# Kernel optimization log

Measured on AMD Instinct MI355X. Metric: run time of the kernel, lower is better.

## Reference

```python
import jax, jax.numpy as jnp
import numpy as np

IN_CH = 32
OUT_CH = 32
M1, M2 = 32, 32
BS, H, W = 8, 256, 256


def setup_inputs() -> dict:
    key = jax.random.key(0)
    kx, kk = jax.random.split(key)
    x = jax.random.normal(kx, (BS, IN_CH, H, W), dtype=jnp.float32)
    # reset_parameters: randn * (1/(in_ch*out_ch)) + 1
    scale = 1.0 / (IN_CH * OUT_CH)
    kernel = jax.random.normal(kk, (2, 1, OUT_CH, M1, M2, 2), dtype=jnp.float32) * scale + 1.0
    r = jnp.float32(1.0)
    return {"x": x, "kernel": kernel, "r": r}


def reference(x, kernel, r):
    # view_as_complex: last dim of 2 -> complex, shape [2, 1, C, M1, M2]
    kc = (kernel[..., 0] + 1j * kernel[..., 1]).astype(jnp.complex64)
    # elementwise complex power kernel**r
    kc = jnp.power(kc, r)

    # forward 2D real FFT over spatial dims (ortho norm)
    x_ft = jnp.fft.rfftn(x, axes=(-2, -1), norm="ortho")  # [bs, C, H, W//2+1]
    Hf, Wr = x_ft.shape[-2], x_ft.shape[-1]
    n1 = min(Hf // 2, M1)
    n2 = min(Wr, M2)

    def mix(block, k):
        # fft over channel dim (-3), multiply by complex kernel, ifft back
        b = jnp.fft.fft(block, axis=-3, norm="ortho")
        b = b * k[..., :n1, :n2]
        return jnp.fft.ifft(b, axis=-3, norm="ortho")

    pos = mix(x_ft[..., :n1, :n2], kc[0])          # low positive freqs
    neg = mix(x_ft[..., Hf - n1:, :n2], kc[1])     # low negative freqs

    out_ft = jnp.zeros((x.shape[0], OUT_CH, Hf, Wr), dtype=jnp.complex64)
    out_ft = out_ft.at[..., :n1, :n2].set(pos)
    out_ft = out_ft.at[..., Hf - n1:, :n2].set(neg)

    # inverse real FFT back to spatial domain
    return jnp.fft.irfftn(out_ft, s=(x.shape[-2], x.shape[-1]), axes=(-2, -1), norm="ortho")
```

## Files before the change

kernel.cpp:

```cpp
#include <hip/hip_runtime.h>
#include <math.h>


#define TWO_PI 6.28318530717958647692f

__global__ __launch_bounds__(256) void kP(const float* __restrict__ kin,
                                          const float* __restrict__ rp,
                                          float2* __restrict__ kp) {
  const int i = blockIdx.x * 256 + threadIdx.x;
  const float r = rp[0];
  const float kr = kin[2 * i], ki = kin[2 * i + 1];
  const float m2 = fmaf(kr, kr, ki * ki);
  float2 o = make_float2(0.f, 0.f);
  if (m2 > 0.f) {
    const float lm = 0.5f * logf(m2);
    const float ang = atan2f(ki, kr);
    const float mag = expf(r * lm);
    float s, c;
    sincosf(r * ang, &s, &c);
    o = make_float2(mag * c, mag * s);
  }
  kp[i] = o;
}

__global__ __launch_bounds__(256) void kA(const float* __restrict__ x,
                                          float2* __restrict__ z1) {
  __shared__ float xs[8192];
  const int tid = threadIdx.x;
  const long row0 = (long)blockIdx.x * 32;
  const float* xg = x + row0 * 256;
  {
    const int xl = tid & 31, rq = tid >> 5;
    const float* xgr = xg + rq * 4 * 256 + xl;
#pragma unroll
    for (int cb = 0; cb < 8; ++cb) {
      const int xc = xl + 32 * cb;
      const float4 v = make_float4(xgr[32 * cb], xgr[32 * cb + 256],
                                   xgr[32 * cb + 512], xgr[32 * cb + 768]);
      *(float4*)(xs + xc * 32 + 4 * ((rq + xc) & 7)) = v;
    }
  }
  __syncthreads();
  const float RT = 0.70710678118654752440f;
#pragma unroll
  for (int k = 0; k < 4; ++k) {
    const int i = tid + (k << 8);
    const int x1 = i >> 5, r = i & 31;
    float* base = xs + x1 * 32 + ((r + 4 * x1) & 31);
    const float a0 = base[0],        a1 = base[1024],     a2 = base[2048];
    const float a3 = base[3 * 1024], a4 = base[4 * 1024], a5 = base[5 * 1024];
    const float a6 = base[6 * 1024], a7 = base[7 * 1024];
    const float t0 = a0 + a4, t1 = a0 - a4, t2 = a2 + a6, t3 = a2 - a6;
    const float u0 = a1 + a5, u1 = a1 - a5, u2 = a3 + a7, u3 = a3 - a7;
    const float E0 = t0 + t2, O0 = u0 + u2;
    const float d1 = RT * (u1 - u3), d2 = RT * (u1 + u3);
    base[0]        = E0 + O0;
    base[1024]     = E0 - O0;
    base[2 * 1024] = t1 + d1;
    base[3 * 1024] = -(t3 + d2);
    base[4 * 1024] = t0 - t2;
    base[5 * 1024] = -(u0 - u2);
    base[6 * 1024] = t1 - d1;
    base[7 * 1024] = t3 - d2;
  }
  __syncthreads();
  const int w = tid & 31;
  const int r0 = (tid >> 5) << 2;
  const int p = w & 7;
  int pr, pi;
  float si;
  if (p == 0)      { pr = 0;           pi = 0;      si = 0.f; }
  else if (p == 4) { pr = 1;           pi = 1;      si = 0.f; }
  else if (p < 4)  { pr = 2 * p;       pi = pr + 1; si = 1.f; }
  else             { pr = 2 * (8 - p); pi = pr + 1; si = -1.f; }
  const char* ur = (const char*)xs + pr * 4096;
  const char* ui = (const char*)xs + pi * 4096;
  const char* urp[8];
  const char* uip[8];
#pragma unroll
  for (int j = 0; j < 8; ++j) {
    const int off = 4 * ((r0 + 4 * j) & 31) + 128 * j;
    urp[j] = ur + off;
    uip[j] = ui + off;
  }
  float s1, c1;
  sincosf(-TWO_PI * (float)w / 256.0f, &s1, &c1);
  float pc = 1.f, ps = 0.f;
  float Cr0 = 0, Cr1 = 0, Cr2 = 0, Cr3 = 0;
  float Ci0 = 0, Ci1 = 0, Ci2 = 0, Ci3 = 0;
#pragma unroll
  for (int bq = 0; bq < 4; ++bq) {
#pragma unroll
    for (int j = 0; j < 8; ++j) {
      const float4 Fr = *(const float4*)(urp[j] + bq * 1024);
      const float4 Fi = *(const float4*)(uip[j] + bq * 1024);
      const float qs = si * ps, qc = si * pc;
      Cr0 = fmaf(Fr.x, pc, fmaf(-Fi.x, qs, Cr0));
      Ci0 = fmaf(Fr.x, ps, fmaf( Fi.x, qc, Ci0));
      Cr1 = fmaf(Fr.y, pc, fmaf(-Fi.y, qs, Cr1));
      Ci1 = fmaf(Fr.y, ps, fmaf( Fi.y, qc, Ci1));
      Cr2 = fmaf(Fr.z, pc, fmaf(-Fi.z, qs, Cr2));
      Ci2 = fmaf(Fr.z, ps, fmaf( Fi.z, qc, Ci2));
      Cr3 = fmaf(Fr.w, pc, fmaf(-Fi.w, qs, Cr3));
      Ci3 = fmaf(Fr.w, ps, fmaf( Fi.w, qc, Ci3));
      const float tn = fmaf(pc, c1, -ps * s1);
      ps = fmaf(pc, s1, ps * c1);
      pc = tn;
    }
  }
  float2* o = z1 + (row0 + r0) * 32 + w;
  o[0]  = make_float2(Cr0, Ci0);
  o[32] = make_float2(Cr1, Ci1);
  o[64] = make_float2(Cr2, Ci2);
  o[96] = make_float2(Cr3, Ci3);
}

__global__ __launch_bounds__(256) void kB1(float2* __restrict__ z1) {
  const int gt = blockIdx.x * 256 + threadIdx.x;
  const int w = gt & 31, y1 = (gt >> 5) & 31, bc = gt >> 10;
  float2* base = z1 + (long)bc * 8192 + y1 * 32 + w;
  float2 a[8];
#pragma unroll
  for (int j = 0; j < 8; ++j) a[j] = base[j * 1024];
  float2 t0 = make_float2(a[0].x + a[4].x, a[0].y + a[4].y);
  float2 t1 = make_float2(a[0].x - a[4].x, a[0].y - a[4].y);
  float2 t2 = make_float2(a[2].x + a[6].x, a[2].y + a[6].y);
  float2 t3 = make_float2(a[2].x - a[6].x, a[2].y - a[6].y);
  const float2 E0 = make_float2(t0.x + t2.x, t0.y + t2.y);
  const float2 E2 = make_float2(t0.x - t2.x, t0.y - t2.y);
  const float2 E1 = make_float2(t1.x + t3.y, t1.y - t3.x);
  const float2 E3 = make_float2(t1.x - t3.y, t1.y + t3.x);
  t0 = make_float2(a[1].x + a[5].x, a[1].y + a[5].y);
  t1 = make_float2(a[1].x - a[5].x, a[1].y - a[5].y);
  t2 = make_float2(a[3].x + a[7].x, a[3].y + a[7].y);
  t3 = make_float2(a[3].x - a[7].x, a[3].y - a[7].y);
  const float2 O0 = make_float2(t0.x + t2.x, t0.y + t2.y);
  const float2 O2 = make_float2(t0.x - t2.x, t0.y - t2.y);
  const float2 O1 = make_float2(t1.x + t3.y, t1.y - t3.x);
  const float2 O3 = make_float2(t1.x - t3.y, t1.y + t3.x);
  const float RT = 0.70710678118654752440f;
  const float2 B0 = O0;
  const float2 B1 = make_float2(RT * (O1.x + O1.y), RT * (O1.y - O1.x));
  const float2 B2 = make_float2(O2.y, -O2.x);
  const float2 B3 = make_float2(RT * (O3.y - O3.x), -RT * (O3.x + O3.y));
  base[0]        = make_float2(E0.x + B0.x, E0.y + B0.y);
  base[1 * 1024] = make_float2(E1.x + B1.x, E1.y + B1.y);
  base[2 * 1024] = make_float2(E2.x + B2.x, E2.y + B2.y);
  base[3 * 1024] = make_float2(E3.x + B3.x, E3.y + B3.y);
  base[4 * 1024] = make_float2(E0.x - B0.x, E0.y - B0.y);
  base[5 * 1024] = make_float2(E1.x - B1.x, E1.y - B1.y);
  base[6 * 1024] = make_float2(E2.x - B2.x, E2.y - B2.y);
  base[7 * 1024] = make_float2(E3.x - B3.x, E3.y - B3.y);
}

__global__ __launch_bounds__(256) void kB2(const float2* __restrict__ s,
                                           float2* __restrict__ z2) {
  const int bc = blockIdx.x >> 3, tq = blockIdx.x & 7;
  const int k = threadIdx.x >> 5, w = threadIdx.x & 31;
  const int t = tq * 8 + k;
  const int h = (t < 32) ? t : (192 + t);
  float sr, cr;
  sincosf(-TWO_PI * (float)h / 256.0f, &sr, &cr);
  const float2* src = s + (long)bc * 8192 + k * 1024 + w;
  float ar = 0.f, ai = 0.f;
  float pc = 1.f, ps = 0.f;
  for (int y1 = 0; y1 < 32; ++y1) {
    const float2 v = src[y1 * 32];
    ar = fmaf(v.x, pc, fmaf(-v.y, ps, ar));
    ai = fmaf(v.x, ps, fmaf( v.y, pc, ai));
    const float tn = fmaf(pc, cr, -ps * sr);
    ps = fmaf(pc, sr, ps * cr);
    pc = tn;
  }
  z2[(long)bc * 2048 + t * 32 + w] = make_float2(ar, ai);
}

__global__ __launch_bounds__(256) void kC(const float2* __restrict__ z2,
                                          const float2* __restrict__ kp,
                                          float2* __restrict__ g) {
  __shared__ float2 z2s[8 * 33];
  __shared__ float2 fk[8 * 33];
  __shared__ float2 tw[32];
  const int tid = threadIdx.x;
  if (tid < 32) {
    float s, c;
    sincosf(-TWO_PI * (float)tid / 32.0f, &s, &c);
    tw[tid] = make_float2(c, s);
  }
  const int m0 = blockIdx.x * 8;
  const int b = m0 >> 11;
  const int twi = m0 & 2047;
  const int t = twi >> 5;
  const int w0 = twi & 31;
  const int s_ = t >> 5, tm = t & 31;
  {
    const int ci = tid >> 3, wj = tid & 7;
    z2s[wj * 33 + ci] = z2[((long)(b * 32 + ci)) * 2048 + t * 32 + w0 + wj];
  }
  __syncthreads();
  const int m = tid & 7;
  {
    const int cf = tid >> 3;
    float fr = 0, fi = 0;
    int i0 = 0;
#pragma unroll 8
    for (int ci = 0; ci < 32; ++ci) {
      const float2 z = z2s[m * 33 + ci];
      const float2 t0 = tw[i0]; i0 = (i0 + cf) & 31;
      fr = fmaf(z.x, t0.x, fmaf(-z.y, t0.y, fr));
      fi = fmaf(z.x, t0.y, fmaf( z.y, t0.x, fi));
    }
    const float2 k0 = kp[((s_ * 32 + cf) * 32 + tm) * 32 + w0 + m];
    fk[m * 33 + cf] = make_float2(fr * k0.x - fi * k0.y, fr * k0.y + fi * k0.x);
  }
  __syncthreads();
  {
    const int co = tid >> 3;
    float gr = 0, gi = 0;
    int i0 = 0;
#pragma unroll 8
    for (int cf = 0; cf < 32; ++cf) {
      const float2 f = fk[m * 33 + cf];
      const float2 t0 = tw[i0]; i0 = (i0 + co) & 31;
      gr = fmaf(f.x, t0.x, fmaf( f.y, t0.y, gr));
      gi = fmaf(f.y, t0.x, fmaf(-f.x, t0.y, gi));
    }
    const float SC = 1.0f / 8192.0f;
    g[((long)(b * 32 + co)) * 2048 + t * 32 + w0 + m] = make_float2(gr * SC, gi * SC);
  }
}

__global__ __launch_bounds__(256) void kD1(const float2* __restrict__ g,
                                           float2* __restrict__ U) {
  const int bc = blockIdx.x >> 3, y1q = blockIdx.x & 7;
  const int p = threadIdx.x >> 5, w = threadIdx.x & 31;
  const float2* gb = g + (long)bc * 2048 + w;
  float2* ub = U + (long)bc * 8192 + p * 32 + w;
#pragma unroll
  for (int y1l = 0; y1l < 4; ++y1l) {
    const int y1 = y1q * 4 + y1l;
    float st, ct;
    sincosf(TWO_PI * (float)y1 / 32.0f, &st, &ct);
    float s1, c1;
    sincosf(TWO_PI * (float)((p * y1) & 255) / 256.0f, &s1, &c1);
    float s2, c2;
    sincosf(TWO_PI * (float)(((224 + p) * y1) & 255) / 256.0f, &s2, &c2);
    float ar = 0.f, ai = 0.f;
    float pc = c1, ps = s1, qc = c2, qs = s2;
#pragma unroll
    for (int j = 0; j < 4; ++j) {
      const float2 va = gb[(p + 8 * j) * 32];
      const float2 vb = gb[(32 + p + 8 * j) * 32];
      ar = fmaf(va.x, pc, fmaf(-va.y, ps, ar));
      ai = fmaf(va.x, ps, fmaf( va.y, pc, ai));
      ar = fmaf(vb.x, qc, fmaf(-vb.y, qs, ar));
      ai = fmaf(vb.x, qs, fmaf( vb.y, qc, ai));
      const float tn = fmaf(pc, ct, -ps * st);
      ps = fmaf(pc, st, ps * ct);
      pc = tn;
      const float tm2 = fmaf(qc, ct, -qs * st);
      qs = fmaf(qc, st, qs * ct);
      qc = tm2;
    }
    ub[y1 * 256] = make_float2(ar, ai);
  }
}

__global__ __launch_bounds__(256) void kDE(const float2* __restrict__ U,
                                           float* __restrict__ out) {
  __shared__ float2 tst[32 * 34];
  const int tid = threadIdx.x;
  const int bc = blockIdx.x >> 3, yq = blockIdx.x & 7;
  {
    const int y5 = tid >> 3, wq = tid & 7;
    const float* ub = (const float*)(U + (long)bc * 8192 + (long)y5 * 256 + wq * 4);
    float Tr[4] = {0.f, 0.f, 0.f, 0.f}, Ti[4] = {0.f, 0.f, 0.f, 0.f};
#pragma unroll
    for (int p = 0; p < 8; ++p) {
      float sp, cp;
      sincosf(TWO_PI * (float)((p * yq) & 7) / 8.0f, &sp, &cp);
      const float4 qa = *(const float4*)(ub + p * 64);
      const float4 qb = *(const float4*)(ub + p * 64 + 4);
      Tr[0] = fmaf(qa.x, cp, fmaf(-qa.y, sp, Tr[0]));
      Ti[0] = fmaf(qa.x, sp, fmaf( qa.y, cp, Ti[0]));
      Tr[1] = fmaf(qa.z, cp, fmaf(-qa.w, sp, Tr[1]));
      Ti[1] = fmaf(qa.z, sp, fmaf( qa.w, cp, Ti[1]));
      Tr[2] = fmaf(qb.x, cp, fmaf(-qb.y, sp, Tr[2]));
      Ti[2] = fmaf(qb.x, sp, fmaf( qb.y, cp, Ti[2]));
      Tr[3] = fmaf(qb.z, cp, fmaf(-qb.w, sp, Tr[3]));
      Ti[3] = fmaf(qb.z, sp, fmaf( qb.w, cp, Ti[3]));
    }
#pragma unroll
    for (int kk = 0; kk < 4; ++kk) {
      const int w = wq * 4 + kk;
      const float sc = w ? (2.0f / 256.0f) : (1.0f / 256.0f);
      tst[w * 34 + y5] = make_float2(Tr[kk] * sc, Ti[kk] * sc);
    }
  }
  __syncthreads();
  {
    const int xq = tid & 31;
    const int rh = tid >> 5;
    float sb, cb;
    sincosf(TWO_PI * (float)xq / 256.0f, &sb, &cb);
    const float RT = 0.70710678118654752440f;
    const float stc1 = RT * (cb - sb), sts1 = RT * (cb + sb);
    const float stc[4] = {cb, stc1, -sb, -sts1};
    const float sts[4] = {sb, sts1, cb, stc1};
    float C[4][4], S[4][4];
#pragma unroll
    for (int m = 0; m < 4; ++m)
#pragma unroll
      for (int j = 0; j < 4; ++j) { C[m][j] = 0.f; S[m][j] = 0.f; }
    float pc[4] = {1.f, 1.f, 1.f, 1.f}, ps[4] = {0.f, 0.f, 0.f, 0.f};
    const float* tbse = (const float*)tst + rh * 8;
#pragma unroll 2
    for (int w = 0; w < 32; ++w) {
      const float4 q0 = *(const float4*)(tbse + w * 68);
      const float4 q1 = *(const float4*)(tbse + w * 68 + 4);
#pragma unroll
      for (int m = 0; m < 4; ++m) {
        C[m][0] = fmaf(q0.x, pc[m], C[m][0]);
        S[m][0] = fmaf(q0.y, ps[m], S[m][0]);
        C[m][1] = fmaf(q0.z, pc[m], C[m][1]);
        S[m][1] = fmaf(q0.w, ps[m], S[m][1]);
        C[m][2] = fmaf(q1.x, pc[m], C[m][2]);
        S[m][2] = fmaf(q1.y, ps[m], S[m][2]);
        C[m][3] = fmaf(q1.z, pc[m], C[m][3]);
        S[m][3] = fmaf(q1.w, ps[m], S[m][3]);
        const float tn = fmaf(pc[m], stc[m], -ps[m] * sts[m]);
        ps[m] = fmaf(pc[m], sts[m], ps[m] * stc[m]);
        pc[m] = tn;
      }
    }
    const long rbase = (long)bc * 256 + yq * 32;
#pragma unroll
    for (int m = 0; m < 4; ++m) {
      const int xx = xq + 32 * m;
#pragma unroll
      for (int j = 0; j < 4; ++j) {
        const long row = rbase + rh * 4 + j;
        out[row * 256 + xx] = C[m][j] - S[m][j];
        out[row * 256 + ((256 - xx) & 255)] = C[m][j] + S[m][j];
      }
    }
    if (tid < 32) {
      float ae = 0.f, ao = 0.f;
#pragma unroll
      for (int k = 0; k < 16; ++k) {
        ae += tst[(2 * k) * 34 + tid].x;
        ao += tst[(2 * k + 1) * 34 + tid].x;
      }
      out[(rbase + tid) * 256 + 128] = ae - ao;
    }
  }
}

extern "C" void kernel_launch(void* const* d_in, const int* in_sizes, int n_in,
                              void* d_out, int out_size, void* d_ws, size_t ws_size,
                              hipStream_t stream) {
  const float* x = (const float*)d_in[0];
  const float* kin = (const float*)d_in[1];
  const float* rp = (const float*)d_in[2];
  float* out = (float*)d_out;
  char* ws = (char*)d_ws;

  float2* z1 = (float2*)(ws);
  float2* z2 = (float2*)(ws + (16ull << 20));
  float2* kp = (float2*)(ws + (24ull << 20));
  float2* g  = (float2*)(ws);
  float2* U  = (float2*)(ws + (4ull << 20));

  kP<<<256, 256, 0, stream>>>(kin, rp, kp);
  kA<<<2048, 256, 0, stream>>>(x, z1);
  kB1<<<1024, 256, 0, stream>>>(z1);
  kB2<<<2048, 256, 0, stream>>>(z1, z2);
  kC<<<2048, 256, 0, stream>>>(z2, kp, g);
  kD1<<<2048, 256, 0, stream>>>(g, U);
  kDE<<<2048, 256, 0, stream>>>(U, out);
}
```

Before: 202.9 us.

## Split row DFT into radix-8 butterfly pass and truncated twiddle pass

```diff
diff --git a/kernel.cpp b/kernel.cpp
--- a/kernel.cpp
+++ b/kernel.cpp
@@ -21,6 +21,101 @@
     o = make_float2(mag * c, mag * s);
   }
   kp[i] = o;
+}
+
+__global__ __launch_bounds__(256) void kA1(const float* __restrict__ x,
+                                           float* __restrict__ F) {
+  const int tid = threadIdx.x;
+  const int x1 = tid & 31, rr = tid >> 5;
+  const long rb = blockIdx.x;
+  const float* xb = x + rb * 32 * 256 + x1;
+  float* Fb = F + rb * 8192 + x1;
+  const float RT = 0.70710678118654752440f;
+#pragma unroll
+  for (int k = 0; k < 4; ++k) {
+    const int rl = rr + 8 * k;
+    const float* xr = xb + rl * 256;
+    const float a0 = xr[0],   a1 = xr[32],  a2 = xr[64],  a3 = xr[96];
+    const float a4 = xr[128], a5 = xr[160], a6 = xr[192], a7 = xr[224];
+    const float t0 = a0 + a4, t1 = a0 - a4, t2 = a2 + a6, t3 = a2 - a6;
+    const float u0 = a1 + a5, u1 = a1 - a5, u2 = a3 + a7, u3 = a3 - a7;
+    const float E0 = t0 + t2, O0 = u0 + u2;
+    const float d1 = RT * (u1 - u3), d2 = RT * (u1 + u3);
+    float* Fo = Fb + rl * 32;
+    Fo[0]        = E0 + O0;
+    Fo[1024]     = E0 - O0;
+    Fo[2 * 1024] = t1 + d1;
+    Fo[3 * 1024] = -(t3 + d2);
+    Fo[4 * 1024] = t0 - t2;
+    Fo[5 * 1024] = -(u0 - u2);
+    Fo[6 * 1024] = t1 - d1;
+    Fo[7 * 1024] = t3 - d2;
+  }
+}
+
+__global__ __launch_bounds__(256) void kA2(const float* __restrict__ F,
+                                           float2* __restrict__ z1) {
+  const int tid = threadIdx.x;
+  const int w = tid & 31, rq = tid >> 5;
+  const long rb = blockIdx.x;
+  const int p = w & 7;
+  int pr, pi;
+  float si;
+  if (p == 0)      { pr = 0;           pi = 0;      si = 0.f; }
+  else if (p == 4) { pr = 1;           pi = 1;      si = 0.f; }
+  else if (p < 4)  { pr = 2 * p;       pi = pr + 1; si = 1.f; }
+  else             { pr = 2 * (8 - p); pi = pr + 1; si = -1.f; }
+  const float* Fr_ = F + rb * 8192 + pr * 1024 + rq * 128;
+  const float* Fi_ = F + rb * 8192 + pi * 1024 + rq * 128;
+  float s1, c1;
+  sincosf(-TWO_PI * (float)w / 256.0f, &s1, &c1);
+  float Pc[4], Ps[4];
+  Pc[0] = 1.f; Ps[0] = 0.f;
+  Pc[1] = c1;  Ps[1] = s1;
+  Pc[2] = fmaf(c1, c1, -s1 * s1);
+  Ps[2] = 2.f * c1 * s1;
+  Pc[3] = fmaf(Pc[2], c1, -Ps[2] * s1);
+  Ps[3] = fmaf(Pc[2], s1, Ps[2] * c1);
+  const float c4 = fmaf(Pc[3], c1, -Ps[3] * s1);
+  const float s4 = fmaf(Pc[3], s1, Ps[3] * c1);
+  float Cr[4] = {0.f, 0.f, 0.f, 0.f}, Ci[4] = {0.f, 0.f, 0.f, 0.f};
+#pragma unroll
+  for (int j = 0; j < 8; ++j) {
+    float4 fr[4], fi[4];
+#pragma unroll
+    for (int r = 0; r < 4; ++r) {
+      fr[r] = *(const float4*)(Fr_ + r * 32 + 4 * j);
+      fi[r] = *(const float4*)(Fi_ + r * 32 + 4 * j);
+    }
+    const float qs0 = si * Ps[0], qc0 = si * Pc[0];
+    const float qs1 = si * Ps[1], qc1 = si * Pc[1];
+    const float qs2 = si * Ps[2], qc2 = si * Pc[2];
+    const float qs3 = si * Ps[3], qc3 = si * Pc[3];
+#pragma unroll
+    for (int r = 0; r < 4; ++r) {
+      float cr = Cr[r], ci = Ci[r];
+      cr = fmaf(fr[r].x, Pc[0], fmaf(-fi[r].x, qs0, cr));
+      ci = fmaf(fr[r].x, Ps[0], fmaf( fi[r].x, qc0, ci));
+      cr = fmaf(fr[r].y, Pc[1], fmaf(-fi[r].y, qs1, cr));
+      ci = fmaf(fr[r].y, Ps[1], fmaf( fi[r].y, qc1, ci));
+      cr = fmaf(fr[r].z, Pc[2], fmaf(-fi[r].z, qs2, cr));
+      ci = fmaf(fr[r].z, Ps[2], fmaf( fi[r].z, qc2, ci));
+      cr = fmaf(fr[r].w, Pc[3], fmaf(-fi[r].w, qs3, cr));
+      ci = fmaf(fr[r].w, Ps[3], fmaf( fi[r].w, qc3, ci));
+      Cr[r] = cr; Ci[r] = ci;
+    }
+#pragma unroll
+    for (int m = 0; m < 4; ++m) {
+      const float tn = fmaf(Pc[m], c4, -Ps[m] * s4);
+      Ps[m] = fmaf(Pc[m], s4, Ps[m] * c4);
+      Pc[m] = tn;
+    }
+  }
+  float2* o = z1 + (rb * 32 + 4 * rq) * 32 + w;
+  o[0]  = make_float2(Cr[0], Ci[0]);
+  o[32] = make_float2(Cr[1], Ci[1]);
+  o[64] = make_float2(Cr[2], Ci[2]);
+  o[96] = make_float2(Cr[3], Ci[3]);
 }
 
 __global__ __launch_bounds__(256) void kA(const float* __restrict__ x,
@@ -365,17 +460,33 @@
   float* out = (float*)d_out;
   char* ws = (char*)d_ws;
 
-  float2* z1 = (float2*)(ws);
-  float2* z2 = (float2*)(ws + (16ull << 20));
-  float2* kp = (float2*)(ws + (24ull << 20));
-  float2* g  = (float2*)(ws);
-  float2* U  = (float2*)(ws + (4ull << 20));
-
-  kP<<<256, 256, 0, stream>>>(kin, rp, kp);
-  kA<<<2048, 256, 0, stream>>>(x, z1);
-  kB1<<<1024, 256, 0, stream>>>(z1);
-  kB2<<<2048, 256, 0, stream>>>(z1, z2);
-  kC<<<2048, 256, 0, stream>>>(z2, kp, g);
-  kD1<<<2048, 256, 0, stream>>>(g, U);
-  kDE<<<2048, 256, 0, stream>>>(U, out);
-}
+  if (ws_size >= (110ull << 20)) {
+    float*  F  = (float*)(ws);
+    float2* z1 = (float2*)(ws + (64ull << 20));
+    float2* z2 = (float2*)(ws + (80ull << 20));
+    float2* kp = (float2*)(ws + (88ull << 20));
+    float2* g  = (float2*)(ws + (89ull << 20));
+    float2* U  = (float2*)(ws + (93ull << 20));
+    kP<<<256, 256, 0, stream>>>(kin, rp, kp);
+    kA1<<<2048, 256, 0, stream>>>(x, F);
+    kA2<<<2048, 256, 0, stream>>>(F, z1);
+    kB1<<<1024, 256, 0, stream>>>(z1);
+    kB2<<<2048, 256, 0, stream>>>(z1, z2);
+    kC<<<2048, 256, 0, stream>>>(z2, kp, g);
+    kD1<<<2048, 256, 0, stream>>>(g, U);
+    kDE<<<2048, 256, 0, stream>>>(U, out);
+  } else {
+    float2* z1 = (float2*)(ws);
+    float2* z2 = (float2*)(ws + (16ull << 20));
+    float2* kp = (float2*)(ws + (24ull << 20));
+    float2* g  = (float2*)(ws);
+    float2* U  = (float2*)(ws + (4ull << 20));
+    kP<<<256, 256, 0, stream>>>(kin, rp, kp);
+    kA<<<2048, 256, 0, stream>>>(x, z1);
+    kB1<<<1024, 256, 0, stream>>>(z1);
+    kB2<<<2048, 256, 0, stream>>>(z1, z2);
+    kC<<<2048, 256, 0, stream>>>(z2, kp, g);
+    kD1<<<2048, 256, 0, stream>>>(g, U);
+    kDE<<<2048, 256, 0, stream>>>(U, out);
+  }
+}
```

New measurement: 261.8 us. 29.0% more time.

## Fuse radix-8 and DFT stages into LDS kernels, merge inverse stages

Applied to the files above, without the earlier changes.

```diff
diff --git a/kernel.cpp b/kernel.cpp
--- a/kernel.cpp
+++ b/kernel.cpp
@@ -115,64 +115,79 @@
   o[96] = make_float2(Cr3, Ci3);
 }
 
-__global__ __launch_bounds__(256) void kB1(float2* __restrict__ z1) {
-  const int gt = blockIdx.x * 256 + threadIdx.x;
-  const int w = gt & 31, y1 = (gt >> 5) & 31, bc = gt >> 10;
-  float2* base = z1 + (long)bc * 8192 + y1 * 32 + w;
-  float2 a[8];
-#pragma unroll
-  for (int j = 0; j < 8; ++j) a[j] = base[j * 1024];
-  float2 t0 = make_float2(a[0].x + a[4].x, a[0].y + a[4].y);
-  float2 t1 = make_float2(a[0].x - a[4].x, a[0].y - a[4].y);
-  float2 t2 = make_float2(a[2].x + a[6].x, a[2].y + a[6].y);
-  float2 t3 = make_float2(a[2].x - a[6].x, a[2].y - a[6].y);
-  const float2 E0 = make_float2(t0.x + t2.x, t0.y + t2.y);
-  const float2 E2 = make_float2(t0.x - t2.x, t0.y - t2.y);
-  const float2 E1 = make_float2(t1.x + t3.y, t1.y - t3.x);
-  const float2 E3 = make_float2(t1.x - t3.y, t1.y + t3.x);
-  t0 = make_float2(a[1].x + a[5].x, a[1].y + a[5].y);
-  t1 = make_float2(a[1].x - a[5].x, a[1].y - a[5].y);
-  t2 = make_float2(a[3].x + a[7].x, a[3].y + a[7].y);
-  t3 = make_float2(a[3].x - a[7].x, a[3].y - a[7].y);
-  const float2 O0 = make_float2(t0.x + t2.x, t0.y + t2.y);
-  const float2 O2 = make_float2(t0.x - t2.x, t0.y - t2.y);
-  const float2 O1 = make_float2(t1.x + t3.y, t1.y - t3.x);
-  const float2 O3 = make_float2(t1.x - t3.y, t1.y + t3.x);
+__global__ __launch_bounds__(256) void kB(const float2* __restrict__ z1,
+                                          float2* __restrict__ z2) {
+  __shared__ float2 zs[8192];
+  const int tid = threadIdx.x;
+  const int bc = blockIdx.x >> 1, th = blockIdx.x & 1;
+  {
+    const float4* s4 = (const float4*)(z1 + (long)bc * 8192);
+    float4* d4 = (float4*)zs;
+    for (int i = tid; i < 4096; i += 256) d4[i] = s4[i];
+  }
+  __syncthreads();
   const float RT = 0.70710678118654752440f;
-  const float2 B0 = O0;
-  const float2 B1 = make_float2(RT * (O1.x + O1.y), RT * (O1.y - O1.x));
-  const float2 B2 = make_float2(O2.y, -O2.x);
-  const float2 B3 = make_float2(RT * (O3.y - O3.x), -RT * (O3.x + O3.y));
-  base[0]        = make_float2(E0.x + B0.x, E0.y + B0.y);
-  base[1 * 1024] = make_float2(E1.x + B1.x, E1.y + B1.y);
-  base[2 * 1024] = make_float2(E2.x + B2.x, E2.y + B2.y);
-  base[3 * 1024] = make_float2(E3.x + B3.x, E3.y + B3.y);
-  base[4 * 1024] = make_float2(E0.x - B0.x, E0.y - B0.y);
-  base[5 * 1024] = make_float2(E1.x - B1.x, E1.y - B1.y);
-  base[6 * 1024] = make_float2(E2.x - B2.x, E2.y - B2.y);
-  base[7 * 1024] = make_float2(E3.x - B3.x, E3.y - B3.y);
-}
-
-__global__ __launch_bounds__(256) void kB2(const float2* __restrict__ s,
-                                           float2* __restrict__ z2) {
-  const int bc = blockIdx.x >> 3, tq = blockIdx.x & 7;
-  const int k = threadIdx.x >> 5, w = threadIdx.x & 31;
-  const int t = tq * 8 + k;
-  const int h = (t < 32) ? t : (192 + t);
-  float sr, cr;
-  sincosf(-TWO_PI * (float)h / 256.0f, &sr, &cr);
-  const float2* src = s + (long)bc * 8192 + k * 1024 + w;
-  float ar = 0.f, ai = 0.f;
-  float pc = 1.f, ps = 0.f;
+#pragma unroll
+  for (int e = 0; e < 4; ++e) {
+    float2* base = zs + tid + (e << 8);
+    float2 a[8];
+#pragma unroll
+    for (int j = 0; j < 8; ++j) a[j] = base[j * 1024];
+    float2 t0 = make_float2(a[0].x + a[4].x, a[0].y + a[4].y);
+    float2 t1 = make_float2(a[0].x - a[4].x, a[0].y - a[4].y);
+    float2 t2 = make_float2(a[2].x + a[6].x, a[2].y + a[6].y);
+    float2 t3 = make_float2(a[2].x - a[6].x, a[2].y - a[6].y);
+    const float2 E0 = make_float2(t0.x + t2.x, t0.y + t2.y);
+    const float2 E2 = make_float2(t0.x - t2.x, t0.y - t2.y);
+    const float2 E1 = make_float2(t1.x + t3.y, t1.y - t3.x);
+    const float2 E3 = make_float2(t1.x - t3.y, t1.y + t3.x);
+    t0 = make_float2(a[1].x + a[5].x, a[1].y + a[5].y);
+    t1 = make_float2(a[1].x - a[5].x, a[1].y - a[5].y);
+    t2 = make_float2(a[3].x + a[7].x, a[3].y + a[7].y);
+    t3 = make_float2(a[3].x - a[7].x, a[3].y - a[7].y);
+    const float2 O0 = make_float2(t0.x + t2.x, t0.y + t2.y);
+    const float2 O2 = make_float2(t0.x - t2.x, t0.y - t2.y);
+    const float2 O1 = make_float2(t1.x + t3.y, t1.y - t3.x);
+    const float2 O3 = make_float2(t1.x - t3.y, t1.y + t3.x);
+    const float2 B0 = O0;
+    const float2 B1 = make_float2(RT * (O1.x + O1.y), RT * (O1.y - O1.x));
+    const float2 B2 = make_float2(O2.y, -O2.x);
+    const float2 B3 = make_float2(RT * (O3.y - O3.x), -RT * (O3.x + O3.y));
+    base[0]        = make_float2(E0.x + B0.x, E0.y + B0.y);
+    base[1 * 1024] = make_float2(E1.x + B1.x, E1.y + B1.y);
+    base[2 * 1024] = make_float2(E2.x + B2.x, E2.y + B2.y);
+    base[3 * 1024] = make_float2(E3.x + B3.x, E3.y + B3.y);
+    base[4 * 1024] = make_float2(E0.x - B0.x, E0.y - B0.y);
+    base[5 * 1024] = make_float2(E1.x - B1.x, E1.y - B1.y);
+    base[6 * 1024] = make_float2(E2.x - B2.x, E2.y - B2.y);
+    base[7 * 1024] = make_float2(E3.x - B3.x, E3.y - B3.y);
+  }
+  __syncthreads();
+  const int w = tid & 31;
+  const int lt = tid >> 5;
+  const int t0i = th * 32 + lt;
+  const int hbase = th ? (192 + t0i) : t0i;
+  float stc[4], sts[4], pcq[4], psq[4], ar[4], ai[4];
+#pragma unroll
+  for (int q = 0; q < 4; ++q) {
+    sincosf(-TWO_PI * (float)(hbase + 8 * q) / 256.0f, &sts[q], &stc[q]);
+    pcq[q] = 1.f; psq[q] = 0.f; ar[q] = 0.f; ai[q] = 0.f;
+  }
+  const float2* sp = zs + lt * 1024 + w;
   for (int y1 = 0; y1 < 32; ++y1) {
-    const float2 v = src[y1 * 32];
-    ar = fmaf(v.x, pc, fmaf(-v.y, ps, ar));
-    ai = fmaf(v.x, ps, fmaf( v.y, pc, ai));
-    const float tn = fmaf(pc, cr, -ps * sr);
-    ps = fmaf(pc, sr, ps * cr);
-    pc = tn;
-  }
-  z2[(long)bc * 2048 + t * 32 + w] = make_float2(ar, ai);
+    const float2 v = sp[y1 * 32];
+#pragma unroll
+    for (int q = 0; q < 4; ++q) {
+      ar[q] = fmaf(v.x, pcq[q], fmaf(-v.y, psq[q], ar[q]));
+      ai[q] = fmaf(v.x, psq[q], fmaf( v.y, pcq[q], ai[q]));
+      const float tn = fmaf(pcq[q], stc[q], -psq[q] * sts[q]);
+      psq[q] = fmaf(pcq[q], sts[q], psq[q] * stc[q]);
+      pcq[q] = tn;
+    }
+  }
+  float2* dst = z2 + (long)bc * 2048 + t0i * 32 + w;
+#pragma unroll
+  for (int q = 0; q < 4; ++q) dst[q * 256] = make_float2(ar[q], ai[q]);
 }
 
 __global__ __launch_bounds__(256) void kC(const float2* __restrict__ z2,
@@ -230,129 +245,120 @@
   }
 }
 
-__global__ __launch_bounds__(256) void kD1(const float2* __restrict__ g,
-                                           float2* __restrict__ U) {
-  const int bc = blockIdx.x >> 3, y1q = blockIdx.x & 7;
-  const int p = threadIdx.x >> 5, w = threadIdx.x & 31;
-  const float2* gb = g + (long)bc * 2048 + w;
-  float2* ub = U + (long)bc * 8192 + p * 32 + w;
-#pragma unroll
-  for (int y1l = 0; y1l < 4; ++y1l) {
-    const int y1 = y1q * 4 + y1l;
-    float st, ct;
-    sincosf(TWO_PI * (float)y1 / 32.0f, &st, &ct);
-    float s1, c1;
-    sincosf(TWO_PI * (float)((p * y1) & 255) / 256.0f, &s1, &c1);
-    float s2, c2;
-    sincosf(TWO_PI * (float)(((224 + p) * y1) & 255) / 256.0f, &s2, &c2);
-    float ar = 0.f, ai = 0.f;
-    float pc = c1, ps = s1, qc = c2, qs = s2;
-#pragma unroll
-    for (int j = 0; j < 4; ++j) {
-      const float2 va = gb[(p + 8 * j) * 32];
-      const float2 vb = gb[(32 + p + 8 * j) * 32];
-      ar = fmaf(va.x, pc, fmaf(-va.y, ps, ar));
-      ai = fmaf(va.x, ps, fmaf( va.y, pc, ai));
-      ar = fmaf(vb.x, qc, fmaf(-vb.y, qs, ar));
-      ai = fmaf(vb.x, qs, fmaf( vb.y, qc, ai));
-      const float tn = fmaf(pc, ct, -ps * st);
-      ps = fmaf(pc, st, ps * ct);
-      pc = tn;
-      const float tm2 = fmaf(qc, ct, -qs * st);
-      qs = fmaf(qc, st, qs * ct);
-      qc = tm2;
-    }
-    ub[y1 * 256] = make_float2(ar, ai);
-  }
-}
-
-__global__ __launch_bounds__(256) void kDE(const float2* __restrict__ U,
-                                           float* __restrict__ out) {
+__global__ __launch_bounds__(512) void kDE2(const float2* __restrict__ g,
+                                            float* __restrict__ out) {
+  __shared__ float2 gs[2048];
   __shared__ float2 tst[32 * 34];
   const int tid = threadIdx.x;
-  const int bc = blockIdx.x >> 3, yq = blockIdx.x & 7;
-  {
-    const int y5 = tid >> 3, wq = tid & 7;
-    const float* ub = (const float*)(U + (long)bc * 8192 + (long)y5 * 256 + wq * 4);
-    float Tr[4] = {0.f, 0.f, 0.f, 0.f}, Ti[4] = {0.f, 0.f, 0.f, 0.f};
-#pragma unroll
-    for (int p = 0; p < 8; ++p) {
-      float sp, cp;
-      sincosf(TWO_PI * (float)((p * yq) & 7) / 8.0f, &sp, &cp);
-      const float4 qa = *(const float4*)(ub + p * 64);
-      const float4 qb = *(const float4*)(ub + p * 64 + 4);
-      Tr[0] = fmaf(qa.x, cp, fmaf(-qa.y, sp, Tr[0]));
-      Ti[0] = fmaf(qa.x, sp, fmaf( qa.y, cp, Ti[0]));
-      Tr[1] = fmaf(qa.z, cp, fmaf(-qa.w, sp, Tr[1]));
-      Ti[1] = fmaf(qa.z, sp, fmaf( qa.w, cp, Ti[1]));
-      Tr[2] = fmaf(qb.x, cp, fmaf(-qb.y, sp, Tr[2]));
-      Ti[2] = fmaf(qb.x, sp, fmaf( qb.y, cp, Ti[2]));
-      Tr[3] = fmaf(qb.z, cp, fmaf(-qb.w, sp, Tr[3]));
-      Ti[3] = fmaf(qb.z, sp, fmaf( qb.w, cp, Ti[3]));
-    }
-#pragma unroll
-    for (int kk = 0; kk < 4; ++kk) {
-      const int w = wq * 4 + kk;
-      const float sc = w ? (2.0f / 256.0f) : (1.0f / 256.0f);
-      tst[w * 34 + y5] = make_float2(Tr[kk] * sc, Ti[kk] * sc);
-    }
-  }
-  __syncthreads();
-  {
-    const int xq = tid & 31;
-    const int rh = tid >> 5;
-    float sb, cb;
-    sincosf(TWO_PI * (float)xq / 256.0f, &sb, &cb);
-    const float RT = 0.70710678118654752440f;
-    const float stc1 = RT * (cb - sb), sts1 = RT * (cb + sb);
-    const float stc[4] = {cb, stc1, -sb, -sts1};
-    const float sts[4] = {sb, sts1, cb, stc1};
-    float C[4][4], S[4][4];
-#pragma unroll
-    for (int m = 0; m < 4; ++m)
-#pragma unroll
-      for (int j = 0; j < 4; ++j) { C[m][j] = 0.f; S[m][j] = 0.f; }
-    float pc[4] = {1.f, 1.f, 1.f, 1.f}, ps[4] = {0.f, 0.f, 0.f, 0.f};
-    const float* tbse = (const float*)tst + rh * 8;
+  const int bc = blockIdx.x >> 1, yh = blockIdx.x & 1;
+  {
+    const float4* s4 = (const float4*)(g + (long)bc * 2048);
+    float4* d4 = (float4*)gs;
+    for (int i = tid; i < 1024; i += 512) d4[i] = s4[i];
+  }
+  __syncthreads();
+  const int w = tid & 31;
+  float Ur[2][8], Ui[2][8];
+#pragma unroll
+  for (int e = 0; e < 2; ++e) {
+    const int y1 = (tid + (e << 9)) >> 5;
+#pragma unroll
+    for (int p = 0; p < 8; ++p) { Ur[e][p] = 0.f; Ui[e][p] = 0.f; }
+    float s1, c1;
+    sincosf(TWO_PI * (float)y1 / 256.0f, &s1, &c1);
+    float pc = 1.f, ps = 0.f;
+#pragma unroll
+    for (int t = 0; t < 64; ++t) {
+      if (t == 32) {
+        float s2, c2;
+        sincosf(TWO_PI * (float)((224 * y1) & 255) / 256.0f, &s2, &c2);
+        pc = c2; ps = s2;
+      }
+      const float2 v = gs[t * 32 + w];
+      const int k = t & 7;
+      Ur[e][k] = fmaf(v.x, pc, fmaf(-v.y, ps, Ur[e][k]));
+      Ui[e][k] = fmaf(v.x, ps, fmaf( v.y, pc, Ui[e][k]));
+      const float tn = fmaf(pc, c1, -ps * s1);
+      ps = fmaf(pc, s1, ps * c1);
+      pc = tn;
+    }
+  }
+  const int xq = tid & 31;
+  const int rh = tid >> 5;
+  float sb, cb;
+  sincosf(TWO_PI * (float)xq / 256.0f, &sb, &cb);
+  const float RT = 0.70710678118654752440f;
+  const float stc1 = RT * (cb - sb), sts1 = RT * (cb + sb);
+  const float stcx[4] = {cb, stc1, -sb, -sts1};
+  const float stsx[4] = {sb, sts1, cb, stc1};
+  const long rb0 = (long)bc * 256;
+#pragma unroll
+  for (int yql = 0; yql < 4; ++yql) {
+    const int yq = yh * 4 + yql;
+    {
+      float sqv, cqv;
+      sincosf(TWO_PI * (float)yq / 8.0f, &sqv, &cqv);
+#pragma unroll
+      for (int e = 0; e < 2; ++e) {
+        const int y1 = (tid + (e << 9)) >> 5;
+        float tr = 0.f, ti = 0.f, qc = 1.f, qs = 0.f;
+#pragma unroll
+        for (int p = 0; p < 8; ++p) {
+          tr = fmaf(Ur[e][p], qc, fmaf(-Ui[e][p], qs, tr));
+          ti = fmaf(Ur[e][p], qs, fmaf( Ui[e][p], qc, ti));
+          const float tn = fmaf(qc, cqv, -qs * sqv);
+          qs = fmaf(qc, sqv, qs * cqv);
+          qc = tn;
+        }
+        const float sc = w ? (2.0f / 256.0f) : (1.0f / 256.0f);
+        tst[w * 34 + y1] = make_float2(tr * sc, ti * sc);
+      }
+    }
+    __syncthreads();
+    {
+      float C[4][2], S[4][2];
+#pragma unroll
+      for (int m = 0; m < 4; ++m) {
+        C[m][0] = 0.f; C[m][1] = 0.f; S[m][0] = 0.f; S[m][1] = 0.f;
+      }
+      float pcx[4] = {1.f, 1.f, 1.f, 1.f}, psx[4] = {0.f, 0.f, 0.f, 0.f};
+      const float* tbse = (const float*)tst + rh * 4;
 #pragma unroll 2
-    for (int w = 0; w < 32; ++w) {
-      const float4 q0 = *(const float4*)(tbse + w * 68);
-      const float4 q1 = *(const float4*)(tbse + w * 68 + 4);
+      for (int w2 = 0; w2 < 32; ++w2) {
+        const float4 q0 = *(const float4*)(tbse + w2 * 68);
+#pragma unroll
+        for (int m = 0; m < 4; ++m) {
+          C[m][0] = fmaf(q0.x, pcx[m], C[m][0]);
+          S[m][0] = fmaf(q0.y, psx[m], S[m][0]);
+          C[m][1] = fmaf(q0.z, pcx[m], C[m][1]);
+          S[m][1] = fmaf(q0.w, psx[m], S[m][1]);
+          const float tn = fmaf(pcx[m], stcx[m], -psx[m] * stsx[m]);
+          psx[m] = fmaf(pcx[m], stsx[m], psx[m] * stcx[m]);
+          pcx[m] = tn;
+        }
+      }
+      const long rbase = rb0 + yq * 32;
 #pragma unroll
       for (int m = 0; m < 4; ++m) {
-        C[m][0] = fmaf(q0.x, pc[m], C[m][0]);
-        S[m][0] = fmaf(q0.y, ps[m], S[m][0]);
-        C[m][1] = fmaf(q0.z, pc[m], C[m][1]);
-        S[m][1] = fmaf(q0.w, ps[m], S[m][1]);
-        C[m][2] = fmaf(q1.x, pc[m], C[m][2]);
-        S[m][2] = fmaf(q1.y, ps[m], S[m][2]);
-        C[m][3] = fmaf(q1.z, pc[m], C[m][3]);
-        S[m][3] = fmaf(q1.w, ps[m], S[m][3]);
-        const float tn = fmaf(pc[m], stc[m], -ps[m] * sts[m]);
-        ps[m] = fmaf(pc[m], sts[m], ps[m] * stc[m]);
-        pc[m] = tn;
-      }
-    }
-    const long rbase = (long)bc * 256 + yq * 32;
-#pragma unroll
-    for (int m = 0; m < 4; ++m) {
-      const int xx = xq + 32 * m;
-#pragma unroll
-      for (int j = 0; j < 4; ++j) {
-        const long row = rbase + rh * 4 + j;
-        out[row * 256 + xx] = C[m][j] - S[m][j];
-        out[row * 256 + ((256 - xx) & 255)] = C[m][j] + S[m][j];
-      }
-    }
-    if (tid < 32) {
-      float ae = 0.f, ao = 0.f;
-#pragma unroll
-      for (int k = 0; k < 16; ++k) {
-        ae += tst[(2 * k) * 34 + tid].x;
-        ao += tst[(2 * k + 1) * 34 + tid].x;
-      }
-      out[(rbase + tid) * 256 + 128] = ae - ao;
-    }
+        const int xx = xq + 32 * m;
+#pragma unroll
+        for (int j = 0; j < 2; ++j) {
+          const long row = rbase + rh * 2 + j;
+          out[row * 256 + xx] = C[m][j] - S[m][j];
+          out[row * 256 + ((256 - xx) & 255)] = C[m][j] + S[m][j];
+        }
+      }
+      if (tid < 32) {
+        float ae = 0.f, ao = 0.f;
+#pragma unroll
+        for (int k = 0; k < 16; ++k) {
+          ae += tst[(2 * k) * 34 + tid].x;
+          ao += tst[(2 * k + 1) * 34 + tid].x;
+        }
+        out[(rbase + tid) * 256 + 128] = ae - ao;
+      }
+    }
+    __syncthreads();
   }
 }
 
@@ -369,13 +375,10 @@
   float2* z2 = (float2*)(ws + (16ull << 20));
   float2* kp = (float2*)(ws + (24ull << 20));
   float2* g  = (float2*)(ws);
-  float2* U  = (float2*)(ws + (4ull << 20));
 
   kP<<<256, 256, 0, stream>>>(kin, rp, kp);
   kA<<<2048, 256, 0, stream>>>(x, z1);
-  kB1<<<1024, 256, 0, stream>>>(z1);
-  kB2<<<2048, 256, 0, stream>>>(z1, z2);
+  kB<<<512, 256, 0, stream>>>(z1, z2);
   kC<<<2048, 256, 0, stream>>>(z2, kp, g);
-  kD1<<<2048, 256, 0, stream>>>(g, U);
-  kDE<<<2048, 256, 0, stream>>>(U, out);
-}
+  kDE2<<<512, 512, 0, stream>>>(g, out);
+}
```

Result: faster. 197.8 us (-2.5%).
